# Kernel tuning notes

Hardware: AMD Instinct MI355X
Metric: run time of the kernel (lower is better)

## Reference

```python
import jax, jax.numpy as jnp
import numpy as np
from jax import lax

B, C, O, K, L, W = 32, 128, 128, 3, 4096, 1
PAD, DIL = 1, 1


def _conv(x, w, b):
    # x: [B,C,H,W], w: [O,C,K,1] -> [B,O,H,W] (zeros padding, stride 1)
    y = lax.conv_general_dilated(x, w, window_strides=(1, 1),
                                 padding=[(PAD, PAD), (0, 0)],
                                 rhs_dilation=(DIL, 1),
                                 dimension_numbers=('NCHW', 'OIHW', 'NCHW'))
    return y + b[None, :, None, None]


def setup_inputs() -> dict:
    key = jax.random.key(0)
    ks = jax.random.split(key, 6)
    x = jax.random.normal(ks[0], (B, C, L, W), dtype=jnp.float32)
    # offset/modulator convs are zero-init in torch; use small random values to
    # exercise the deformable gather path (represents a trained state)
    w_off = jax.random.normal(ks[1], (2 * K, C, K, 1), dtype=jnp.float32) * 0.01
    b_off = jax.random.normal(ks[2], (2 * K,), dtype=jnp.float32) * 0.1
    w_mod = jax.random.normal(ks[3], (K, C, K, 1), dtype=jnp.float32) * 0.01
    b_mod = jax.random.normal(ks[4], (K,), dtype=jnp.float32) * 0.1
    w_reg = jax.random.normal(ks[5], (O, C, K, 1), dtype=jnp.float32) * (1.0 / np.sqrt(C * K))
    return {"x": x, "w_off": w_off, "b_off": b_off,
            "w_mod": w_mod, "b_mod": b_mod, "w_reg": w_reg}


def reference(x, w_off, b_off, w_mod, b_mod, w_reg):
    b, c, h, w = x.shape
    max_offset = max(h, w) / 4.0
    offset = jnp.clip(_conv(x, w_off, b_off), -max_offset, max_offset)  # [B,2K,H,W]
    mask = 2.0 * jax.nn.sigmoid(_conv(x, w_mod, b_mod))                 # [B,K,H,W]

    off = offset.reshape(b, K, 2, h, w)
    off_y, off_x = off[:, :, 0], off[:, :, 1]                           # [B,K,H,W]

    # sampling positions (stride=1, pad_w=0, kw=1)
    base_y = (-PAD + jnp.arange(K, dtype=jnp.float32)[:, None] * DIL
              + jnp.arange(h, dtype=jnp.float32)[None, :])              # [K,H]
    py = base_y[None, :, :, None] + off_y                               # [B,K,H,W]
    px = jnp.arange(w, dtype=jnp.float32)[None, None, None, :] + off_x  # [B,K,H,W]

    y0 = jnp.floor(py); x0 = jnp.floor(px)
    iy0 = y0.astype(jnp.int32); ix0 = x0.astype(jnp.int32)
    wy1 = py - y0; wy0 = 1.0 - wy1
    wx1 = px - x0; wx0 = 1.0 - wx1

    def gather(iy, ix):
        iyc = jnp.clip(iy, 0, h - 1)
        ixc = jnp.clip(ix, 0, w - 1)
        # per-batch gather: xb [C,H,W], idx [K,H,W] -> [C,K,H,W]
        return jax.vmap(lambda xb, yb, xb_i: xb[:, yb, xb_i])(x, iyc, ixc)

    acc = jnp.zeros((b, c, K, h, w), dtype=x.dtype)
    corners = [(iy0, ix0, wy0 * wx0), (iy0, ix0 + 1, wy0 * wx1),
               (iy0 + 1, ix0, wy1 * wx0), (iy0 + 1, ix0 + 1, wy1 * wx1)]
    for iy, ix, wgt in corners:
        valid = ((iy >= 0) & (iy < h) & (ix >= 0) & (ix < w)).astype(x.dtype)
        acc = acc + gather(iy, ix) * (wgt * valid)[:, None]  # [B,C,K,H,W]

    val = acc * mask[:, None]                                 # modulated samples
    out = jnp.einsum('bckhw,ock->bohw', val, w_reg[:, :, :, 0])
    return out
```

## Files before the change

### kernel.cpp

```cpp
#include <hip/hip_runtime.h>
#include <hip/hip_bf16.h>
#include <math.h>


typedef __attribute__((ext_vector_type(8))) short bf16x8;
typedef __attribute__((ext_vector_type(4))) float f32x4;
typedef float f32x2u __attribute__((ext_vector_type(2), aligned(4)));

#define WIN 160
#define WPAD 161

static __device__ inline unsigned short f2bf(float f) {
    __hip_bfloat16 h = __float2bfloat16(f);
    union { __hip_bfloat16 b; unsigned short u; } cv;
    cv.b = h;
    return cv.u;
}

__global__ __launch_bounds__(256) void k_wra(const float* __restrict__ w_reg,
                                             const float* __restrict__ w_off,
                                             const float* __restrict__ w_mod,
                                             unsigned short* __restrict__ WrA,
                                             float* __restrict__ wT) {
    int t = blockIdx.x * 256 + threadIdx.x;
    if (t < 8 * 12 * 64 * 8) {
        int e  = t & 7;
        int l  = (t >> 3) & 63;
        int ms = t >> 9;
        int m  = ms / 12;
        int s  = ms - m * 12;
        int o  = m * 16 + (l & 15);
        int kc = s * 32 + ((l >> 4) & 3) * 8 + e;
        int tap = kc >> 7;
        int c   = kc & 127;
        WrA[t] = f2bf(w_reg[(o * 128 + c) * 3 + tap]);
    } else if (t < 8 * 12 * 64 * 8 + 128 * 27) {
        int u = t - 8 * 12 * 64 * 8;
        int c = u / 27, r = u - c * 27;
        int ch = r / 3, tap = r - ch * 3;
        wT[c * 32 + r] = (ch < 6) ? w_off[(ch * 128 + c) * 3 + tap]
                                  : w_mod[((ch - 6) * 128 + c) * 3 + tap];
    }
}

__global__ __launch_bounds__(512) void k_prep(const float* __restrict__ x,
                                              const float* __restrict__ wT,
                                              const float* __restrict__ b_off,
                                              const float* __restrict__ b_mod,
                                              int* __restrict__ addr2,
                                              float* __restrict__ wae,
                                              float* __restrict__ wbe) {
    __shared__ float red[7 * 64 * 19];
    int t = threadIdx.x;
    int lane = t & 63;
    int wv = t >> 6;
    int b = blockIdx.y;
    int i = blockIdx.x * 128 + lane * 2;

    int c0 = __builtin_amdgcn_readfirstlane(wv) * 16;

    float acc[18];
#pragma unroll
    for (int z = 0; z < 18; ++z) acc[z] = 0.f;

    const float* xr = x + (size_t)b * 524288 + (size_t)c0 * 4096;
    const float* wbase = wT + c0 * 32;
#pragma unroll 2
    for (int c = 0; c < 16; ++c) {
        const float* row = xr + (size_t)c * 4096;
        f32x2u v = *(const f32x2u*)(row + i);
        float lm = row[max(i - 1, 0)];
        float rp = row[min(i + 2, 4095)];
        float left  = (i > 0)        ? lm : 0.f;
        float right = (i + 2 < 4096) ? rp : 0.f;
        const float* wrow = wbase + c * 32;
#pragma unroll
        for (int ch = 0; ch < 9; ++ch) {
            float w0 = wrow[ch * 3 + 0];
            float w1 = wrow[ch * 3 + 1];
            float w2 = wrow[ch * 3 + 2];
            acc[ch * 2 + 0] += left * w0 + v.x * w1 + v.y  * w2;
            acc[ch * 2 + 1] += v.x  * w0 + v.y * w1 + right * w2;
        }
    }

    if (wv > 0) {
        float* r = &red[((wv - 1) * 64 + lane) * 19];
#pragma unroll
        for (int z = 0; z < 18; ++z) r[z] = acc[z];
    }
    __syncthreads();
    if (wv != 0) return;

#pragma unroll
    for (int p = 0; p < 7; ++p) {
        const float* r = &red[(p * 64 + lane) * 19];
#pragma unroll
        for (int z = 0; z < 18; ++z) acc[z] += r[z];
    }

#pragma unroll
    for (int k = 0; k < 3; ++k) {
        int   av[2];
        float wav[2], wbv[2];
#pragma unroll
        for (int ii = 0; ii < 2; ++ii) {
            float offy = acc[(2 * k) * 2 + ii]     + b_off[2 * k];
            float offx = acc[(2 * k + 1) * 2 + ii] + b_off[2 * k + 1];
            offy = fminf(fmaxf(offy, -1024.f), 1024.f);
            offx = fminf(fmaxf(offx, -1024.f), 1024.f);
            float am = acc[(6 + k) * 2 + ii] + b_mod[k];
            float m  = 2.f / (1.f + expf(-am));

            float py = (float)(i + ii - 1 + k) + offy;
            float y0 = floorf(py);
            int   iy0 = (int)y0;
            float wy1 = py - y0, wy0 = 1.f - wy1;
            float x0f = floorf(offx);
            int   ix0 = (int)x0f;
            float wx1 = offx - x0f, wx0 = 1.f - wx1;

            float sx = (ix0 == 0) ? wx0 : ((ix0 == -1) ? wx1 : 0.f);
            float scal = m * sx;

            float wAv = (iy0 >= 0 && iy0 < 4096)  ? scal * wy0 : 0.f;
            float wBv = (iy0 >= -1 && iy0 < 4095) ? scal * wy1 : 0.f;

            int addr = min(max(iy0, 0), 4094);
            bool eq = (iy0 == addr);
            wav[ii] = eq ? wAv : (iy0 == -1   ? wBv : 0.f);
            wbv[ii] = eq ? wBv : (iy0 == 4095 ? wAv : 0.f);
            av[ii] = addr;
        }
        int j = (b * 3 + k) * 4096 + i;
        *(int2*)(addr2 + j)  = make_int2(av[0], av[1]);
        *(f32x2u*)(wae + j)  = (f32x2u){wav[0], wav[1]};
        *(f32x2u*)(wbe + j)  = (f32x2u){wbv[0], wbv[1]};
    }
}

__global__ __launch_bounds__(512) void k_fused(const unsigned short* __restrict__ WrA,
                                               const float* __restrict__ x,
                                               const int* __restrict__ addr2,
                                               const float* __restrict__ wae,
                                               const float* __restrict__ wbe,
                                               float* __restrict__ out) {
    __shared__ float win[32 * WPAD];
    __shared__ short Bl[2][8][3][512];
    int t = threadIdx.x;
    int l = t & 63;
    int w = t >> 6;
    int b  = blockIdx.y;
    int ib = blockIdx.x;
    int q = l >> 4;
    int il = l & 15;
    int mg = w & 3;
    int hh = w >> 2;
    int i0t = ib * 128;
    int i0p = i0t + w * 16 + il;
    int wsod = i0t - 16;
    if (wsod > 4096 - WIN) wsod = 4096 - WIN;
    if (wsod < 0) wsod = 0;
    const float* xb = x + (size_t)b * 524288;
    const bf16x8* Ag = (const bf16x8*)WrA;

    int   a_[3];
    float wa_[3], wb_[3];
    bool  okw[3];
#pragma unroll
    for (int k = 0; k < 3; ++k) {
        int j = (b * 3 + k) * 4096 + i0p;
        int a = addr2[j];
        a_[k]  = a;
        wa_[k] = wae[j];
        wb_[k] = wbe[j];
        okw[k] = (bool)__all(a >= wsod && a <= wsod + WIN - 2);
    }

    f32x4 acc[2][4];
#pragma unroll
    for (int mm = 0; mm < 2; ++mm)
#pragma unroll
        for (int ff = 0; ff < 4; ++ff) acc[mm][ff] = (f32x4){0.f, 0.f, 0.f, 0.f};

#pragma unroll
    for (int it = 0; it < 3; ++it) {
        int idx = it * 512 + t;
        if (idx < 1280) {
            int r  = idx / 40;
            int cp = idx - r * 40;
            float4 v = *(const float4*)(xb + (size_t)r * 4096 + wsod + cp * 4);
            float* dst = &win[r * WPAD + cp * 4];
            dst[0] = v.x; dst[1] = v.y; dst[2] = v.z; dst[3] = v.w;
        }
    }
    __syncthreads();

    for (int cc = 0; cc < 4; ++cc) {
        int p  = cc & 1;
        int cb = cc * 32;

        bf16x8 Areg[2][3];
#pragma unroll
        for (int mm = 0; mm < 2; ++mm)
#pragma unroll
            for (int k = 0; k < 3; ++k)
                Areg[mm][k] = Ag[((mg * 2 + mm) * 12 + k * 4 + cc) * 64 + l];

#pragma unroll
        for (int k = 0; k < 3; ++k) {
            float v[8];
            float wa = wa_[k], wb = wb_[k];
            if (okw[k]) {
                int pos = a_[k] - wsod;
#pragma unroll
                for (int e = 0; e < 8; ++e) {
                    const float* base = &win[(q * 8 + e) * WPAD + pos];
                    v[e] = wa * base[0] + wb * base[1];
                }
            } else {
                int a = a_[k];
#pragma unroll
                for (int e = 0; e < 8; ++e) {
                    const float* row = xb + (size_t)(cb + q * 8 + e) * 4096;
                    f32x2u p2 = *(const f32x2u*)(row + a);
                    v[e] = wa * p2.x + wb * p2.y;
                }
            }
            bf16x8 Bv;
#pragma unroll
            for (int e = 0; e < 8; ++e) Bv[e] = (short)f2bf(v[e]);
            *(bf16x8*)&Bl[p][w][k][l * 8] = Bv;
        }

        float4 stg[3];
        if (cc < 3) {
            const float* src = xb + (size_t)(cb + 32) * 4096;
#pragma unroll
            for (int it = 0; it < 3; ++it) {
                int idx = it * 512 + t;
                if (idx < 1280) {
                    int r  = idx / 40;
                    int cp = idx - r * 40;
                    stg[it] = *(const float4*)(src + (size_t)r * 4096 + wsod + cp * 4);
                }
            }
        }
        __syncthreads();

        __builtin_amdgcn_s_setprio(1);
#pragma unroll
        for (int ff = 0; ff < 4; ++ff) {
            int f = hh * 4 + ff;
#pragma unroll
            for (int k = 0; k < 3; ++k) {
                bf16x8 Bv = *(const bf16x8*)&Bl[p][f][k][l * 8];
                acc[0][ff] = __builtin_amdgcn_mfma_f32_16x16x32_bf16(Areg[0][k], Bv, acc[0][ff], 0, 0, 0);
                acc[1][ff] = __builtin_amdgcn_mfma_f32_16x16x32_bf16(Areg[1][k], Bv, acc[1][ff], 0, 0, 0);
            }
        }
        __builtin_amdgcn_s_setprio(0);

        if (cc < 3) {
#pragma unroll
            for (int it = 0; it < 3; ++it) {
                int idx = it * 512 + t;
                if (idx < 1280) {
                    int r  = idx / 40;
                    int cp = idx - r * 40;
                    float* dst = &win[r * WPAD + cp * 4];
                    dst[0] = stg[it].x; dst[1] = stg[it].y;
                    dst[2] = stg[it].z; dst[3] = stg[it].w;
                }
            }
            __syncthreads();
        }
    }

    int r0 = q * 4;
#pragma unroll
    for (int mm = 0; mm < 2; ++mm) {
#pragma unroll
        for (int ff = 0; ff < 4; ++ff) {
#pragma unroll
            for (int r = 0; r < 4; ++r) {
                int o = (mg * 2 + mm) * 16 + r0 + r;
                out[((size_t)(b * 128 + o)) * 4096 + i0t + (hh * 4 + ff) * 16 + il] = acc[mm][ff][r];
            }
        }
    }
}

extern "C" void kernel_launch(void* const* d_in, const int* in_sizes, int n_in,
                              void* d_out, int out_size, void* d_ws, size_t ws_size,
                              hipStream_t stream) {
    const float* x     = (const float*)d_in[0];
    const float* w_off = (const float*)d_in[1];
    const float* b_off = (const float*)d_in[2];
    const float* w_mod = (const float*)d_in[3];
    const float* b_mod = (const float*)d_in[4];
    const float* w_reg = (const float*)d_in[5];
    float* out = (float*)d_out;

    char* ws = (char*)d_ws;
    unsigned short* WrA = (unsigned short*)(ws);
    float* wT    = (float*)(ws + 98304);
    int*   addr2 = (int*)  (ws + 131072);
    float* wae   = (float*)(ws + 1703936);
    float* wbe   = (float*)(ws + 3276800);

    k_wra<<<206, 256, 0, stream>>>(w_reg, w_off, w_mod, WrA, wT);
    k_prep<<<dim3(32, 32), 512, 0, stream>>>(x, wT, b_off, b_mod,
                                             addr2, wae, wbe);
    k_fused<<<dim3(32, 32), 512, 0, stream>>>(WrA, x, addr2, wae, wbe, out);
}
```

Measured before the change: 78.49 us.

## Store LDS window as packed bf16 neighbor pairs and use lighter barriers

Result: no change. 77.12 us (-1.7%).

```diff
diff --git a/kernel.cpp b/kernel.cpp
--- a/kernel.cpp
+++ b/kernel.cpp
@@ -8,13 +8,16 @@
 typedef float f32x2u __attribute__((ext_vector_type(2), aligned(4)));
 
 #define WIN 160
-#define WPAD 161
+#define WP32 162
 
 static __device__ inline unsigned short f2bf(float f) {
     __hip_bfloat16 h = __float2bfloat16(f);
     union { __hip_bfloat16 b; unsigned short u; } cv;
     cv.b = h;
     return cv.u;
+}
+static __device__ inline unsigned pk2(float a, float b) {
+    return (unsigned)f2bf(a) | ((unsigned)f2bf(b) << 16);
 }
 
 __global__ __launch_bounds__(256) void k_wra(const float* __restrict__ w_reg,
@@ -145,8 +148,8 @@
                                                const float* __restrict__ wae,
                                                const float* __restrict__ wbe,
                                                float* __restrict__ out) {
-    __shared__ float win[32 * WPAD];
-    __shared__ short Bl[2][8][3][512];
+    __shared__ unsigned win32[32 * WP32];
+    __shared__ short Bl[8][3][512];
     int t = threadIdx.x;
     int l = t & 63;
     int w = t >> 6;
@@ -164,6 +167,17 @@
     const float* xb = x + (size_t)b * 524288;
     const bf16x8* Ag = (const bf16x8*)WrA;
 
+    int  rr_[3], cp_[3];
+    bool v_[3];
+#pragma unroll
+    for (int it = 0; it < 3; ++it) {
+        int idx = it * 512 + t;
+        int r = idx / 40;
+        rr_[it] = r;
+        cp_[it] = idx - r * 40;
+        v_[it]  = (idx < 1280);
+    }
+
     int   a_[3];
     float wa_[3], wb_[3];
     bool  okw[3];
@@ -185,19 +199,19 @@
 
 #pragma unroll
     for (int it = 0; it < 3; ++it) {
-        int idx = it * 512 + t;
-        if (idx < 1280) {
-            int r  = idx / 40;
-            int cp = idx - r * 40;
-            float4 v = *(const float4*)(xb + (size_t)r * 4096 + wsod + cp * 4);
-            float* dst = &win[r * WPAD + cp * 4];
-            dst[0] = v.x; dst[1] = v.y; dst[2] = v.z; dst[3] = v.w;
+        if (v_[it]) {
+            const float* row = xb + (size_t)rr_[it] * 4096;
+            int c0 = wsod + cp_[it] * 4;
+            float4 v = *(const float4*)(row + c0);
+            float nx = row[min(c0 + 4, 4095)];
+            unsigned* d = &win32[rr_[it] * WP32 + cp_[it] * 4];
+            *(uint2*)(d)     = make_uint2(pk2(v.x, v.y), pk2(v.y, v.z));
+            *(uint2*)(d + 2) = make_uint2(pk2(v.z, v.w), pk2(v.w, nx));
         }
     }
     __syncthreads();
 
     for (int cc = 0; cc < 4; ++cc) {
-        int p  = cc & 1;
         int cb = cc * 32;
 
         bf16x8 Areg[2][3];
@@ -215,8 +229,10 @@
                 int pos = a_[k] - wsod;
 #pragma unroll
                 for (int e = 0; e < 8; ++e) {
-                    const float* base = &win[(q * 8 + e) * WPAD + pos];
-                    v[e] = wa * base[0] + wb * base[1];
+                    unsigned u = win32[(q * 8 + e) * WP32 + pos];
+                    float lo = __uint_as_float(u << 16);
+                    float hi = __uint_as_float(u & 0xffff0000u);
+                    v[e] = wa * lo + wb * hi;
                 }
             } else {
                 int a = a_[k];
@@ -230,23 +246,26 @@
             bf16x8 Bv;
 #pragma unroll
             for (int e = 0; e < 8; ++e) Bv[e] = (short)f2bf(v[e]);
-            *(bf16x8*)&Bl[p][w][k][l * 8] = Bv;
-        }
-
-        float4 stg[3];
+            *(bf16x8*)&Bl[w][k][l * 8] = Bv;
+        }
+
+        float4 sv[3];
+        float  sn[3];
         if (cc < 3) {
-            const float* src = xb + (size_t)(cb + 32) * 4096;
 #pragma unroll
             for (int it = 0; it < 3; ++it) {
-                int idx = it * 512 + t;
-                if (idx < 1280) {
-                    int r  = idx / 40;
-                    int cp = idx - r * 40;
-                    stg[it] = *(const float4*)(src + (size_t)r * 4096 + wsod + cp * 4);
+                if (v_[it]) {
+                    const float* row = xb + (size_t)(cb + 32 + rr_[it]) * 4096;
+                    int c0 = wsod + cp_[it] * 4;
+                    sv[it] = *(const float4*)(row + c0);
+                    sn[it] = row[min(c0 + 4, 4095)];
                 }
             }
         }
-        __syncthreads();
+
+        asm volatile("s_waitcnt lgkmcnt(0)" ::: "memory");
+        __builtin_amdgcn_sched_barrier(0);
+        __builtin_amdgcn_s_barrier();
 
         __builtin_amdgcn_s_setprio(1);
 #pragma unroll
@@ -254,7 +273,7 @@
             int f = hh * 4 + ff;
 #pragma unroll
             for (int k = 0; k < 3; ++k) {
-                bf16x8 Bv = *(const bf16x8*)&Bl[p][f][k][l * 8];
+                bf16x8 Bv = *(const bf16x8*)&Bl[f][k][l * 8];
                 acc[0][ff] = __builtin_amdgcn_mfma_f32_16x16x32_bf16(Areg[0][k], Bv, acc[0][ff], 0, 0, 0);
                 acc[1][ff] = __builtin_amdgcn_mfma_f32_16x16x32_bf16(Areg[1][k], Bv, acc[1][ff], 0, 0, 0);
             }
@@ -264,16 +283,15 @@
         if (cc < 3) {
 #pragma unroll
             for (int it = 0; it < 3; ++it) {
-                int idx = it * 512 + t;
-                if (idx < 1280) {
-                    int r  = idx / 40;
-                    int cp = idx - r * 40;
-                    float* dst = &win[r * WPAD + cp * 4];
-                    dst[0] = stg[it].x; dst[1] = stg[it].y;
-                    dst[2] = stg[it].z; dst[3] = stg[it].w;
+                if (v_[it]) {
+                    unsigned* d = &win32[rr_[it] * WP32 + cp_[it] * 4];
+                    *(uint2*)(d)     = make_uint2(pk2(sv[it].x, sv[it].y), pk2(sv[it].y, sv[it].z));
+                    *(uint2*)(d + 2) = make_uint2(pk2(sv[it].z, sv[it].w), pk2(sv[it].w, sn[it]));
                 }
             }
-            __syncthreads();
+            asm volatile("s_waitcnt lgkmcnt(0)" ::: "memory");
+            __builtin_amdgcn_sched_barrier(0);
+            __builtin_amdgcn_s_barrier();
         }
     }
 
```
